# Performance work log

Measured on AMD Instinct MI355X. Metric: run time of the kernel, lower is better.

Reference implementation:

```python
import jax, jax.numpy as jnp
import numpy as np

EMBED_DIM = 768
NUM_HEADS = 12
LORA_DIM = 64
HEAD_DIM = EMBED_DIM // NUM_HEADS
SCALING = float(HEAD_DIM) ** -0.5


def quick_gelu(x):
    return x * jax.nn.sigmoid(1.702 * x)


def setup_inputs() -> dict:
    key = jax.random.key(0)
    ks = jax.random.split(key, 12)
    bsz, tgt_len, E = 128, 197, EMBED_DIM
    x = jax.random.normal(ks[0], (bsz, tgt_len, E), dtype=jnp.float32)
    attn_mask = jnp.zeros((bsz, tgt_len, tgt_len), dtype=jnp.float32)
    top_idx = jax.random.randint(ks[1], (bsz,), 0, tgt_len)
    s = 0.02
    return {
        "x": x,
        "attn_mask": attn_mask,
        "in_proj_weight": jax.random.normal(ks[2], (3 * E, E)) * s,
        "in_proj_bias": jnp.zeros((3 * E,), jnp.float32),
        "out_proj_weight": jax.random.normal(ks[3], (E, E)) * s,
        "out_proj_bias": jnp.zeros((E,), jnp.float32),
        "lora_a": jax.random.normal(ks[4], (LORA_DIM, E)) * s,
        "lora_b": jax.random.normal(ks[5], (3 * E, LORA_DIM)) * s,
        "down_weight": jax.random.normal(ks[6], (LORA_DIM, E)) * s,
        "down_bias": jax.random.normal(ks[7], (LORA_DIM,)) * 1e-6,
        "up_weight": jax.random.normal(ks[8], (E, LORA_DIM)) * s,
        "up_bias": jnp.zeros((E,), jnp.float32),
        "n_f": 16,
        "top_idx": top_idx,
    }


def reference(x, attn_mask, in_proj_weight, in_proj_bias, out_proj_weight,
              out_proj_bias, lora_a, lora_b, down_weight, down_bias,
              up_weight, up_bias, n_f, top_idx):
    bsz, tgt_len, E = x.shape
    H, hd = NUM_HEADS, HEAD_DIM
    b = bsz // n_f

    # fused QKV + LoRA delta
    qkv = x @ in_proj_weight.T + in_proj_bias          # [bsz, L, 3E]
    qkv = qkv + (x @ lora_a.T) @ lora_b.T              # LoRA delta
    qkv = qkv.reshape(bsz, tgt_len, 3, H, hd)
    qkv = jnp.transpose(qkv, (2, 0, 3, 1, 4))          # [3, bsz, H, L, hd]
    q, k, v = qkv[0], qkv[1], qkv[2]

    # gather per-sample CLS query before scaling (matches torch order)
    q_1 = q[jnp.arange(bsz), :, top_idx, :]            # [bsz, H, hd]
    q_1 = jnp.transpose(q_1.reshape(b, n_f, H, hd), (0, 2, 1, 3))  # [b, H, f, hd]

    # frame-local attention
    attn = jnp.einsum('bhqd,bhkd->bhqk', q * SCALING, k) + attn_mask[:, None, :, :]
    attn = jax.nn.softmax(attn, axis=-1)
    xo = jnp.einsum('bhqk,bhkd->bhqd', attn, v)
    xo = jnp.transpose(xo, (0, 2, 1, 3)).reshape(bsz, tgt_len, E)
    xo = xo @ out_proj_weight.T + out_proj_bias        # [bsz, L, E]

    # global CLS attention over all frames' keys/values
    k_g = jnp.transpose(k.reshape(b, n_f, H, tgt_len, hd), (0, 2, 1, 3, 4)).reshape(b, H, n_f * tgt_len, hd)
    v_g = jnp.transpose(v.reshape(b, n_f, H, tgt_len, hd), (0, 2, 1, 3, 4)).reshape(b, H, n_f * tgt_len, hd)
    mask_g = attn_mask[:, -1, :].reshape(b, n_f * tgt_len)  # [b, f*L]

    attn_1 = jnp.einsum('bhfd,bhkd->bhfk', q_1 * SCALING, k_g) + mask_g[:, None, None, :]
    attn_1 = jax.nn.softmax(attn_1, axis=-1)
    x_1 = jnp.einsum('bhfk,bhkd->bhfd', attn_1, v_g)
    x_1 = jnp.transpose(x_1, (0, 2, 1, 3)).reshape(b, n_f, E)
    x_1 = x_1 @ out_proj_weight.T + out_proj_bias      # [b, f, E]

    # adapter on gathered CLS outputs
    x_0 = xo[jnp.arange(bsz), top_idx, :].reshape(b, n_f, E)
    x_0 = quick_gelu(x_0 @ down_weight.T + down_bias)
    x_0 = x_0 @ up_weight.T + up_bias                  # [b, f, E]

    update_cls = (x_0 + x_1).reshape(bsz, E)
    xo = xo.at[jnp.arange(bsz), top_idx, :].set(update_cls)
    return xo
```

## Files before the change

kernel.cpp:

```cpp
#include <hip/hip_runtime.h>
#include <hip/hip_bf16.h>

typedef __attribute__((ext_vector_type(4))) float f32x4;
typedef __attribute__((ext_vector_type(8))) short s16x8;

#define BSZ 128
#define TGT 197
#define EDIM 768
#define NH 12
#define HD 64
#define NF 16
#define M_TOT (BSZ*TGT)
#define QKV_N (3*EDIM)
#define KG (NF*TGT)
#define KGP 3328
#define VSTR 264

__device__ __forceinline__ float b2f(unsigned short u) {
  return __uint_as_float(((unsigned int)u) << 16);
}
__device__ __forceinline__ float bf2f(__hip_bfloat16 b) { return __bfloat162float(b); }
__device__ __forceinline__ __hip_bfloat16 f2bf(float f) { return __float2bfloat16(f); }
__device__ __forceinline__ unsigned int packbf(float a, float b) {
  __hip_bfloat16 x = __float2bfloat16(a), y = __float2bfloat16(b);
  return (unsigned int)*(unsigned short*)&x | ((unsigned int)*(unsigned short*)&y << 16);
}
__device__ __forceinline__ int swz(int t, int c) {
  return t*64 + (c ^ ((((t & 7) ^ ((t >> 3) & 3))) << 3));
}
__device__ __forceinline__ int vswz(int d, int t) {
  return d*VSTR + (t ^ (d & 56));
}

__device__ __forceinline__ void gload_lds16(const void* gsrc, void* ldst) {
  __builtin_amdgcn_global_load_lds(
      (const __attribute__((address_space(1))) unsigned int*)gsrc,
      (__attribute__((address_space(3))) unsigned int*)ldst, 16, 0, 0);
}

__global__ void detect_dtype(const unsigned short* __restrict__ xraw,
                             int* __restrict__ flag, int* __restrict__ mz) {
  if (threadIdx.x == 0 && blockIdx.x == 0) {
    float mx = 0.f;
    for (int j = 0; j < 1024; ++j) {
      float v = fabsf(b2f(xraw[j]));
      if (v < 1e30f) mx = fmaxf(mx, v);
      else mx = 1e30f;
    }
    *flag = (mx < 100.0f) ? 1 : 0;
    *mz = 1;
  }
}

__global__ __launch_bounds__(256) void detect_mask_zero(
    const unsigned int* __restrict__ mraw, int nelem,
    const int* __restrict__ flag, int* __restrict__ mz)
{
  const int isbf = *flag;
  const int nwords = isbf ? (nelem >> 1) : nelem;
  const unsigned int am = isbf ? 0x7fff7fffu : 0x7fffffffu;
  unsigned int acc = 0;
  for (int i = blockIdx.x*256 + threadIdx.x; i < nwords; i += gridDim.x*256)
    acc |= (mraw[i] & am);
  if (acc) atomicAnd(mz, 0);
}

__global__ __launch_bounds__(256) void convert_bf16(
    const void* __restrict__ src, __hip_bfloat16* __restrict__ dst,
    int n8, const int* __restrict__ flag, int skip_if_bf)
{
  const int isbf = *flag;
  if (skip_if_bf && isbf) return;
  int i = blockIdx.x * 256 + threadIdx.x;
  const int stride = gridDim.x * 256;
  if (isbf) {
    const s16x8* s = (const s16x8*)src;
    s16x8* d = (s16x8*)dst;
    for (; i < n8; i += stride) d[i] = s[i];
  } else {
    const f32x4* s = (const f32x4*)src;
    s16x8* d = (s16x8*)dst;
    for (; i < n8; i += stride) {
      f32x4 a = s[i*2], b = s[i*2+1];
      s16x8 o;
      #pragma unroll
      for (int j = 0; j < 4; ++j) { __hip_bfloat16 t = f2bf(a[j]); o[j] = *(short*)&t; }
      #pragma unroll
      for (int j = 0; j < 4; ++j) { __hip_bfloat16 t = f2bf(b[j]); o[4+j] = *(short*)&t; }
      d[i] = o;
    }
  }
}

__global__ __launch_bounds__(256) void build_wc(
    const __hip_bfloat16* __restrict__ W,
    const __hip_bfloat16* __restrict__ la,
    const __hip_bfloat16* __restrict__ lb,
    __hip_bfloat16* __restrict__ Wc)
{
  __shared__ float lbr[64];
  const int n = blockIdx.x;
  if (threadIdx.x < 64) lbr[threadIdx.x] = bf2f(lb[n*64 + threadIdx.x]);
  __syncthreads();
  for (int e = threadIdx.x; e < EDIM; e += 256) {
    float acc = bf2f(W[(size_t)n*EDIM + e]);
    for (int r = 0; r < 64; ++r) acc += lbr[r] * bf2f(la[r*EDIM + e]);
    Wc[(size_t)n*EDIM + e] = f2bf(acc);
  }
}

__global__ __launch_bounds__(512) void gemm_bt_8ph(
    const __hip_bfloat16* __restrict__ A,
    const __hip_bfloat16* __restrict__ A_alt,
    const __hip_bfloat16* __restrict__ B,
    const __hip_bfloat16* __restrict__ bias,
    void* __restrict__ C,
    int M, int N, int K, int ntiles,
    const int* __restrict__ flag, int flag_mode)
{
  __shared__ char lds[131072];
  const int tid = threadIdx.x;
  const int wave = tid >> 6, lane = tid & 63;
  const int l16 = lane & 15, kq = lane >> 4;
  const int wr = wave >> 2, wc2 = wave & 3;

  const int nwg = gridDim.x;
  const int bid = blockIdx.x;
  const int qc = nwg >> 3, rc = nwg & 7;
  const int xcd = bid & 7;
  const int wgid = (xcd < rc ? xcd*(qc+1) : rc*(qc+1) + (xcd-rc)*qc) + (bid >> 3);
  const long brow = (long)(wgid / ntiles) * 256;
  const long bcol = (long)(wgid % ntiles) * 256;

  const int isbf = *flag;
  const __hip_bfloat16* Ause = isbf ? A_alt : A;
  const int nkt = K >> 6;

  const int srow = tid >> 3;
  const int schunk = tid & 7;
  const int wuni = wave << 10;

  auto stA = [&](int t, int buf, int issue) {
    int ar = issue*64 + srow;
    int cs = schunk ^ (ar & 7);
    long gr = brow + ar; if (gr > (long)M - 1) gr = M - 1;
    gload_lds16(Ause + gr*(long)K + t*64 + cs*8,
                lds + buf*65536 + issue*8192 + wuni);
  };
  auto stB = [&](int t, int buf, int issue) {
    int br = issue*64 + srow;
    int cs = schunk ^ (br & 7);
    gload_lds16(B + (bcol + br)*(long)K + t*64 + cs*8,
                lds + buf*65536 + 32768 + issue*8192 + wuni);
  };
  auto rdA = [&](int buf, int q, int a, int ks) -> s16x8 {
    int ar = wr*128 + q*32 + a*16 + l16;
    int ch = ks*4 + kq;
    return *(const s16x8*)(lds + buf*65536 + ar*128 + ((ch ^ (ar & 7)) << 4));
  };
  auto rdB = [&](int buf, int ni, int ks) -> s16x8 {
    int br = wc2*64 + ni*16 + l16;
    int ch = ks*4 + kq;
    return *(const s16x8*)(lds + buf*65536 + 32768 + br*128 + ((ch ^ (br & 7)) << 4));
  };

  f32x4 acc[8][4];
  #pragma unroll
  for (int i = 0; i < 8; ++i)
    #pragma unroll
    for (int j = 0; j < 4; ++j) acc[i][j] = (f32x4){0.f,0.f,0.f,0.f};

  stB(0,0,0); stB(0,0,1); stB(0,0,2); stB(0,0,3);
  stA(0,0,0); stA(0,0,2); stA(0,0,1); stA(0,0,3);
  asm volatile("s_waitcnt vmcnt(2)" ::: "memory");
  __builtin_amdgcn_s_barrier();

  for (int t = 0; t < nkt; ++t) {
    const int cur = t & 1, nxt = cur ^ 1;
    const bool pf = (t + 1 < nkt);
    s16x8 bfr[4][2], af[2][2];

    #pragma unroll
    for (int ni = 0; ni < 4; ++ni) { bfr[ni][0] = rdB(cur,ni,0); bfr[ni][1] = rdB(cur,ni,1); }
    af[0][0]=rdA(cur,0,0,0); af[0][1]=rdA(cur,0,0,1);
    af[1][0]=rdA(cur,0,1,0); af[1][1]=rdA(cur,0,1,1);
    if (pf) { stB(t+1,nxt,0); stB(t+1,nxt,1); }
    __builtin_amdgcn_s_barrier();
    asm volatile("s_waitcnt lgkmcnt(0)" ::: "memory");
    __builtin_amdgcn_sched_barrier(0);
    __builtin_amdgcn_s_setprio(1);
    #pragma unroll
    for (int ks = 0; ks < 2; ++ks)
      #pragma unroll
      for (int ni = 0; ni < 4; ++ni) {
        acc[0][ni] = __builtin_amdgcn_mfma_f32_16x16x32_bf16(af[0][ks], bfr[ni][ks], acc[0][ni], 0,0,0);
        acc[1][ni] = __builtin_amdgcn_mfma_f32_16x16x32_bf16(af[1][ks], bfr[ni][ks], acc[1][ni], 0,0,0);
      }
    __builtin_amdgcn_s_setprio(0);

    af[0][0]=rdA(cur,1,0,0); af[0][1]=rdA(cur,1,0,1);
    af[1][0]=rdA(cur,1,1,0); af[1][1]=rdA(cur,1,1,1);
    if (pf) {
      stB(t+1,nxt,2); stB(t+1,nxt,3);
      asm volatile("s_waitcnt vmcnt(4)" ::: "memory");
    } else {
      asm volatile("s_waitcnt vmcnt(0)" ::: "memory");
    }
    __builtin_amdgcn_s_barrier();
    asm volatile("s_waitcnt lgkmcnt(0)" ::: "memory");
    __builtin_amdgcn_sched_barrier(0);
    __builtin_amdgcn_s_setprio(1);
    #pragma unroll
    for (int ks = 0; ks < 2; ++ks)
      #pragma unroll
      for (int ni = 0; ni < 4; ++ni) {
        acc[2][ni] = __builtin_amdgcn_mfma_f32_16x16x32_bf16(af[0][ks], bfr[ni][ks], acc[2][ni], 0,0,0);
        acc[3][ni] = __builtin_amdgcn_mfma_f32_16x16x32_bf16(af[1][ks], bfr[ni][ks], acc[3][ni], 0,0,0);
      }
    __builtin_amdgcn_s_setprio(0);

    af[0][0]=rdA(cur,2,0,0); af[0][1]=rdA(cur,2,0,1);
    af[1][0]=rdA(cur,2,1,0); af[1][1]=rdA(cur,2,1,1);
    if (pf) { stA(t+1,nxt,0); stA(t+1,nxt,2); }
    __builtin_amdgcn_s_barrier();
    asm volatile("s_waitcnt lgkmcnt(0)" ::: "memory");
    __builtin_amdgcn_sched_barrier(0);
    __builtin_amdgcn_s_setprio(1);
    #pragma unroll
    for (int ks = 0; ks < 2; ++ks)
      #pragma unroll
      for (int ni = 0; ni < 4; ++ni) {
        acc[4][ni] = __builtin_amdgcn_mfma_f32_16x16x32_bf16(af[0][ks], bfr[ni][ks], acc[4][ni], 0,0,0);
        acc[5][ni] = __builtin_amdgcn_mfma_f32_16x16x32_bf16(af[1][ks], bfr[ni][ks], acc[5][ni], 0,0,0);
      }
    __builtin_amdgcn_s_setprio(0);

    af[0][0]=rdA(cur,3,0,0); af[0][1]=rdA(cur,3,0,1);
    af[1][0]=rdA(cur,3,1,0); af[1][1]=rdA(cur,3,1,1);
    if (pf) { stA(t+1,nxt,1); stA(t+1,nxt,3); }
    asm volatile("s_waitcnt vmcnt(2)" ::: "memory");
    __builtin_amdgcn_s_barrier();
    asm volatile("s_waitcnt lgkmcnt(0)" ::: "memory");
    __builtin_amdgcn_sched_barrier(0);
    __builtin_amdgcn_s_setprio(1);
    #pragma unroll
    for (int ks = 0; ks < 2; ++ks)
      #pragma unroll
      for (int ni = 0; ni < 4; ++ni) {
        acc[6][ni] = __builtin_amdgcn_mfma_f32_16x16x32_bf16(af[0][ks], bfr[ni][ks], acc[6][ni], 0,0,0);
        acc[7][ni] = __builtin_amdgcn_mfma_f32_16x16x32_bf16(af[1][ks], bfr[ni][ks], acc[7][ni], 0,0,0);
      }
    __builtin_amdgcn_s_setprio(0);
  }

  __builtin_amdgcn_s_barrier();

  const int f32o = flag_mode && (!isbf);
  float bv[4];
  #pragma unroll
  for (int ni = 0; ni < 4; ++ni) bv[ni] = bf2f(bias[bcol + wc2*64 + ni*16 + l16]);
  const int o4 = kq*4;

  if (!f32o) {
    __hip_bfloat16* eb = (__hip_bfloat16*)(lds + wave*2048);
    __hip_bfloat16* Cb = (__hip_bfloat16*)C;
    const int rr = lane >> 3, cg = lane & 7;
    #pragma unroll
    for (int mi = 0; mi < 8; ++mi) {
      #pragma unroll
      for (int ni = 0; ni < 4; ++ni)
        #pragma unroll
        for (int r = 0; r < 4; ++r) {
          const int row16 = o4 + r;
          const int sidx = row16*64 + ((((ni*2 + (l16 >> 3)) ^ (row16 & 7)) << 3) | (l16 & 7));
          eb[sidx] = f2bf(acc[mi][ni][r] + bv[ni]);
        }
      asm volatile("s_waitcnt lgkmcnt(0)" ::: "memory");
      __builtin_amdgcn_sched_barrier(0);
      #pragma unroll
      for (int pass = 0; pass < 2; ++pass) {
        const int row16 = pass*8 + rr;
        const long grow = brow + wr*128 + mi*16 + row16;
        if (grow < M) {
          s16x8 v = *(const s16x8*)(eb + row16*64 + ((cg ^ (row16 & 7)) << 3));
          *(s16x8*)(Cb + grow*(long)N + bcol + wc2*64 + cg*8) = v;
        }
      }
      asm volatile("s_waitcnt lgkmcnt(0)" ::: "memory");
      __builtin_amdgcn_sched_barrier(0);
    }
  } else {
    #pragma unroll
    for (int mi = 0; mi < 8; ++mi)
      #pragma unroll
      for (int ni = 0; ni < 4; ++ni)
        #pragma unroll
        for (int r = 0; r < 4; ++r) {
          const long grow = brow + wr*128 + mi*16 + o4 + r;
          if (grow < M)
            ((float*)C)[grow*(long)N + bcol + wc2*64 + ni*16 + l16] = acc[mi][ni][r] + bv[ni];
        }
  }
}

__global__ __launch_bounds__(256) void attn_fused(
    const __hip_bfloat16* __restrict__ qkv,
    const __hip_bfloat16* __restrict__ mask,
    const __hip_bfloat16* __restrict__ mask_raw,
    const int* __restrict__ flag,
    const int* __restrict__ mzp,
    __hip_bfloat16* __restrict__ xop)
{
  __shared__ __hip_bfloat16 lVt[64*VSTR];

  const int tid = threadIdx.x;
  const int blk = blockIdx.x;
  const int xcd = blk & 7;
  const int slot = blk >> 3;
  const int ih = xcd * 192 + (slot >> 2);
  const int qt = slot & 3;
  const int h = ih % NH;
  const int i = ih / NH;
  const int q0 = qt * 64;
  const size_t rowbase = (size_t)i * TGT;
  const int wave = tid >> 6, lane = tid & 63;
  const int l16 = lane & 15, kq = lane >> 4;
  const int mz = *mzp;
  const __hip_bfloat16* msk = (*flag) ? mask_raw : mask;

  int qr = q0 + wave*16 + l16;
  const int qrc = qr > TGT-1 ? TGT-1 : qr;
  s16x8 qf[2];
  #pragma unroll
  for (int kk = 0; kk < 2; ++kk)
    qf[kk] = *(const s16x8*)(qkv + (rowbase + qrc)*QKV_N + h*HD + kk*32 + kq*8);

  const f32x4 z = {0.f,0.f,0.f,0.f};
  for (int idx = tid; idx < 224*8; idx += 256) {
    int t = idx >> 3, c8 = idx & 7;
    f32x4 vv = z;
    if (t < TGT) vv = *(const f32x4*)(qkv + (rowbase + t)*QKV_N + 2*EDIM + h*HD + c8*8);
    const __hip_bfloat16* pv = (const __hip_bfloat16*)&vv;
    const int tx = t ^ (c8 << 3);
    #pragma unroll
    for (int j = 0; j < 8; ++j)
      lVt[(c8*8 + j)*VSTR + tx] = pv[j];
  }
  __syncthreads();

  f32x4 acc[14];
  #pragma unroll
  for (int nf = 0; nf < 14; ++nf) {
    int trow = nf*16 + l16; if (trow > TGT-1) trow = TGT-1;
    acc[nf] = (f32x4){0.f,0.f,0.f,0.f};
    #pragma unroll
    for (int kk = 0; kk < 2; ++kk) {
      s16x8 kf = *(const s16x8*)(qkv + (rowbase + trow)*QKV_N + EDIM + h*HD + kk*32 + kq*8);
      acc[nf] = __builtin_amdgcn_mfma_f32_16x16x32_bf16(kf, qf[kk], acc[nf], 0, 0, 0);
    }
  }

  float mx = -1e30f;
  #pragma unroll
  for (int nf = 0; nf < 14; ++nf) {
    #pragma unroll
    for (int r = 0; r < 4; ++r) {
      const int t = nf*16 + kq*4 + r;
      float s;
      if (t < TGT) {
        s = acc[nf][r]*0.125f;
        if (!mz) s += bf2f(msk[(rowbase + qrc)*TGT + t]);
      } else s = -1e30f;
      acc[nf][r] = s;
      mx = fmaxf(mx, s);
    }
  }
  mx = fmaxf(mx, __shfl_xor(mx, 16));
  mx = fmaxf(mx, __shfl_xor(mx, 32));

  float rs = 0.f;
  unsigned int pk[14][2];
  #pragma unroll
  for (int nf = 0; nf < 14; ++nf) {
    float p0 = __expf(acc[nf][0] - mx);
    float p1 = __expf(acc[nf][1] - mx);
    float p2 = __expf(acc[nf][2] - mx);
    float p3 = __expf(acc[nf][3] - mx);
    rs += (p0 + p1) + (p2 + p3);
    pk[nf][0] = packbf(p0, p1);
    pk[nf][1] = packbf(p2, p3);
  }
  rs += __shfl_xor(rs, 16);
  rs += __shfl_xor(rs, 32);

  f32x4 oacc[4];
  #pragma unroll
  for (int nf = 0; nf < 4; ++nf) oacc[nf] = (f32x4){0.f,0.f,0.f,0.f};

  const int slbase = l16 + ((kq & 1) << 5);
  #pragma unroll
  for (int kt = 0; kt < 7; ++kt) {
    s16x8 pa;
    #pragma unroll
    for (int jp = 0; jp < 4; ++jp) {
      const int srcLane = slbase + ((jp >> 1) << 4);
      int va = __shfl((int)pk[2*kt][jp & 1], srcLane, 64);
      int vb = __shfl((int)pk[2*kt + 1][jp & 1], srcLane, 64);
      int sel = (kq < 2) ? va : vb;
      pa[2*jp]     = (short)(sel & 0xffff);
      pa[2*jp + 1] = (short)(((unsigned int)sel) >> 16);
    }
    #pragma unroll
    for (int nf = 0; nf < 4; ++nf) {
      s16x8 vf = *(const s16x8*)(lVt + vswz(nf*16 + l16, kt*32 + kq*8));
      oacc[nf] = __builtin_amdgcn_mfma_f32_16x16x32_bf16(pa, vf, oacc[nf], 0, 0, 0);
    }
  }

  #pragma unroll
  for (int r = 0; r < 4; ++r) {
    const float rsrc = __shfl(rs, kq*4 + r, 64);
    const int qw = q0 + wave*16 + kq*4 + r;
    if (qw < TGT) {
      const float inv = 1.0f / rsrc;
      #pragma unroll
      for (int nf = 0; nf < 4; ++nf)
        xop[(rowbase + qw)*(size_t)EDIM + h*HD + nf*16 + l16] = f2bf(oacc[nf][r] * inv);
    }
  }
}

__global__ __launch_bounds__(256) void cls_attn(
    const __hip_bfloat16* __restrict__ qkv,
    const __hip_bfloat16* __restrict__ mask,
    const __hip_bfloat16* __restrict__ mask_raw,
    const int* __restrict__ flag,
    const int* __restrict__ mzp,
    const int* __restrict__ top_idx,
    __hip_bfloat16* __restrict__ Sg_all,
    __hip_bfloat16* __restrict__ x1buf)
{
  __shared__ __hip_bfloat16 lQ[16*64];
  __shared__ __hip_bfloat16 lV[256*64];
  __shared__ float red[16][17];
  __shared__ float rmax[16];
  __shared__ float rsum[16];

  const int tid = threadIdx.x;
  const int g = blockIdx.x / NH;
  const int h = blockIdx.x % NH;
  __hip_bfloat16* Sg = Sg_all + (size_t)blockIdx.x * 16 * KGP;
  const int wave = tid >> 6, lane = tid & 63;
  const int l16 = lane & 15, kq = lane >> 4, o4 = (lane >> 4) * 4;
  const int mz = *mzp;
  const __hip_bfloat16* msk = (*flag) ? mask_raw : mask;

  if (tid < 128) {
    int qi = tid >> 3, c8 = tid & 7;
    int ib = g*NF + qi;
    int top = top_idx[ib];
    f32x4 v = *(const f32x4*)(qkv + ((size_t)ib*TGT + top)*QKV_N + h*HD + c8*8);
    *(f32x4*)(lQ + qi*64 + c8*8) = v;
  }
  __syncthreads();

  s16x8 q8[2];
  #pragma unroll
  for (int kk = 0; kk < 2; ++kk)
    q8[kk] = *(const s16x8*)(lQ + l16*64 + kk*32 + kq*8);

  for (int nf = wave; nf < 208; nf += 4) {
    const int key = nf*16 + l16;
    if (nf < 197) {
      f32x4 a = {0.f,0.f,0.f,0.f};
      const size_t krow = (size_t)g*KG + key;
      #pragma unroll
      for (int kk = 0; kk < 2; ++kk) {
        s16x8 k8 = *(const s16x8*)(qkv + krow*QKV_N + EDIM + h*HD + kk*32 + kq*8);
        a = __builtin_amdgcn_mfma_f32_16x16x32_bf16(q8[kk], k8, a, 0, 0, 0);
      }
      float mval = 0.f;
      if (!mz) {
        const int f = key / 197;
        const int t = key - f*197;
        mval = bf2f(msk[((size_t)(g*NF + f)*TGT + (TGT-1))*TGT + t]);
      }
      #pragma unroll
      for (int r = 0; r < 4; ++r)
        Sg[(o4 + r)*KGP + key] = f2bf(a[r]*0.125f + mval);
    } else {
      #pragma unroll
      for (int r = 0; r < 4; ++r)
        Sg[(o4 + r)*KGP + key] = f2bf(0.f);
    }
  }
  __syncthreads();

  {
    const int q = tid >> 4, c = tid & 15;
    float mx = -1e30f;
    for (int gch = c; gch < 394; gch += 16) {
      s16x8 sv = *(const s16x8*)(Sg + q*KGP + gch*8);
      #pragma unroll
      for (int j = 0; j < 8; ++j) mx = fmaxf(mx, b2f((unsigned short)sv[j]));
    }
    red[q][c] = mx;
    __syncthreads();
    if (tid < 16) {
      float m = red[tid][0];
      for (int j = 1; j < 16; ++j) m = fmaxf(m, red[tid][j]);
      rmax[tid] = m;
    }
    __syncthreads();
    const float rowmax = rmax[q];
    float sum = 0.f;
    for (int gch = c; gch < 394; gch += 16) {
      s16x8 sv = *(const s16x8*)(Sg + q*KGP + gch*8);
      s16x8 ov;
      #pragma unroll
      for (int jp = 0; jp < 4; ++jp) {
        float e0 = __expf(b2f((unsigned short)sv[2*jp])   - rowmax);
        float e1 = __expf(b2f((unsigned short)sv[2*jp+1]) - rowmax);
        sum += e0 + e1;
        unsigned int pr = packbf(e0, e1);
        ov[2*jp]   = (short)(pr & 0xffff);
        ov[2*jp+1] = (short)(pr >> 16);
      }
      *(s16x8*)(Sg + q*KGP + gch*8) = ov;
    }
    red[q][c] = sum;
    __syncthreads();
    if (tid < 16) {
      float s = 0.f;
      for (int j = 0; j < 16; ++j) s += red[tid][j];
      rsum[tid] = s;
    }
  }

  f32x4 oa = {0.f,0.f,0.f,0.f};
  const f32x4 z = {0.f,0.f,0.f,0.f};
  for (int ck = 0; ck < KGP; ck += 256) {
    __syncthreads();
    for (int idx = tid; idx < 256*8; idx += 256) {
      int t2 = idx >> 3, c8 = idx & 7;
      int key = ck + t2;
      f32x4 v = z;
      if (key < KG) v = *(const f32x4*)(qkv + ((size_t)g*KG + key)*QKV_N + 2*EDIM + h*HD + c8*8);
      *(f32x4*)(lV + swz(t2, c8*8)) = v;
    }
    __syncthreads();
    #pragma unroll
    for (int ks = 0; ks < 8; ++ks) {
      s16x8 pa = *(const s16x8*)(Sg + l16*KGP + ck + ks*32 + kq*8);
      s16x8 vf;
      #pragma unroll
      for (int j = 0; j < 8; ++j) {
        const int t2 = ks*32 + kq*8 + j;
        vf[j] = *(const short*)(lV + swz(t2, wave*16 + l16));
      }
      oa = __builtin_amdgcn_mfma_f32_16x16x32_bf16(pa, vf, oa, 0, 0, 0);
    }
  }
  #pragma unroll
  for (int r = 0; r < 4; ++r) {
    int q = o4 + r;
    int ib = g*NF + q;
    x1buf[(size_t)ib*EDIM + h*HD + wave*16 + l16] = f2bf(oa[r] / rsum[q]);
  }
}

__global__ __launch_bounds__(256) void final_update(
    void* __restrict__ out,
    const __hip_bfloat16* __restrict__ x1p,
    const __hip_bfloat16* __restrict__ dw, const __hip_bfloat16* __restrict__ db,
    const __hip_bfloat16* __restrict__ uw, const __hip_bfloat16* __restrict__ ub,
    const int* __restrict__ top_idx, const int* __restrict__ flag)
{
  __shared__ float x0[EDIM];
  __shared__ float hmid[64];
  const int i = blockIdx.x;
  const int tid = threadIdx.x;
  const int top = top_idx[i];
  const int isbf = *flag;
  const size_t rowoff = ((size_t)i*TGT + top)*EDIM;
  for (int e = tid; e < EDIM; e += 256)
    x0[e] = isbf ? bf2f(((const __hip_bfloat16*)out)[rowoff + e])
                 : ((const float*)out)[rowoff + e];
  __syncthreads();
  if (tid < 64) {
    float a = bf2f(db[tid]);
    for (int e = 0; e < EDIM; ++e) a += x0[e] * bf2f(dw[tid*EDIM + e]);
    hmid[tid] = a / (1.f + __expf(-1.702f * a));
  }
  __syncthreads();
  for (int e = tid; e < EDIM; e += 256) {
    float a = bf2f(ub[e]) + bf2f(x1p[(size_t)i*EDIM + e]);
    #pragma unroll
    for (int r = 0; r < 64; ++r) a += hmid[r] * bf2f(uw[e*64 + r]);
    if (isbf) ((__hip_bfloat16*)out)[rowoff + e] = f2bf(a);
    else ((float*)out)[rowoff + e] = a;
  }
}

extern "C" void kernel_launch(void* const* d_in, const int* in_sizes, int n_in,
                              void* d_out, int out_size, void* d_ws, size_t ws_size,
                              hipStream_t stream) {
  (void)in_sizes; (void)n_in; (void)out_size; (void)ws_size;
  const int* top_idx = (const int*)d_in[13];
  const __hip_bfloat16* x_raw    = (const __hip_bfloat16*)d_in[0];
  const __hip_bfloat16* mask_raw = (const __hip_bfloat16*)d_in[1];

  char* ws = (char*)d_ws;
  size_t off = 0;
  auto alloc = [&](size_t bytes) { char* p = ws + off; off += (bytes + 15) & ~(size_t)15; return p; };

  int* flag = (int*)alloc(16);
  int* mz   = (int*)alloc(16);
  __hip_bfloat16* x_c    = (__hip_bfloat16*)alloc((size_t)19365888*2);
  __hip_bfloat16* mask_c = (__hip_bfloat16*)alloc((size_t)4967552*2);
  __hip_bfloat16* wIn_c  = (__hip_bfloat16*)alloc((size_t)1769472*2);
  __hip_bfloat16* bIn_c  = (__hip_bfloat16*)alloc((size_t)2304*2);
  __hip_bfloat16* wOut_c = (__hip_bfloat16*)alloc((size_t)589824*2);
  __hip_bfloat16* bOut_c = (__hip_bfloat16*)alloc((size_t)768*2);
  __hip_bfloat16* la_c   = (__hip_bfloat16*)alloc((size_t)49152*2);
  __hip_bfloat16* lb_c   = (__hip_bfloat16*)alloc((size_t)147456*2);
  __hip_bfloat16* dw_c   = (__hip_bfloat16*)alloc((size_t)49152*2);
  __hip_bfloat16* db_c   = (__hip_bfloat16*)alloc((size_t)64*2);
  __hip_bfloat16* uw_c   = (__hip_bfloat16*)alloc((size_t)49152*2);
  __hip_bfloat16* ub_c   = (__hip_bfloat16*)alloc((size_t)768*2);
  __hip_bfloat16* Wc     = (__hip_bfloat16*)alloc((size_t)QKV_N*EDIM*2);
  __hip_bfloat16* qkv    = (__hip_bfloat16*)alloc((size_t)M_TOT*QKV_N*2);
  __hip_bfloat16* xop    = (__hip_bfloat16*)alloc((size_t)M_TOT*EDIM*2);
  __hip_bfloat16* x1b    = (__hip_bfloat16*)alloc((size_t)BSZ*EDIM*2);
  __hip_bfloat16* x1p    = (__hip_bfloat16*)alloc((size_t)BSZ*EDIM*2);
  __hip_bfloat16* Sg     = (__hip_bfloat16*)alloc((size_t)96*16*KGP*2);

  detect_dtype<<<1, 64, 0, stream>>>((const unsigned short*)d_in[0], flag, mz);
  detect_mask_zero<<<2048, 256, 0, stream>>>((const unsigned int*)d_in[1], 4967552, flag, mz);

  auto CV = [&](int idx, __hip_bfloat16* dst, int n, int skip) {
    int n8 = n / 8;
    int grid = (n8 + 255) / 256; if (grid > 2048) grid = 2048; if (grid < 1) grid = 1;
    convert_bf16<<<grid, 256, 0, stream>>>(d_in[idx], dst, n8, flag, skip);
  };
  CV(0,  x_c,    19365888, 1);
  CV(1,  mask_c, 4967552, 1);
  CV(2,  wIn_c,  1769472, 0);
  CV(3,  bIn_c,  2304, 0);
  CV(4,  wOut_c, 589824, 0);
  CV(5,  bOut_c, 768, 0);
  CV(6,  la_c,   49152, 0);
  CV(7,  lb_c,   147456, 0);
  CV(8,  dw_c,   49152, 0);
  CV(9,  db_c,   64, 0);
  CV(10, uw_c,   49152, 0);
  CV(11, ub_c,   768, 0);

  build_wc<<<2304, 256, 0, stream>>>(wIn_c, la_c, lb_c, Wc);

  gemm_bt_8ph<<<99*9, 512, 0, stream>>>(x_c, x_raw, Wc, bIn_c, qkv,
                                        M_TOT, QKV_N, EDIM, 9, flag, 0);
  attn_fused<<<dim3(6144), 256, 0, stream>>>(qkv, mask_c, mask_raw, flag, mz, xop);
  gemm_bt_8ph<<<99*3, 512, 0, stream>>>(xop, xop, wOut_c, bOut_c, d_out,
                                        M_TOT, EDIM, EDIM, 3, flag, 1);
  cls_attn<<<dim3(96), 256, 0, stream>>>(qkv, mask_c, mask_raw, flag, mz, top_idx, Sg, x1b);
  gemm_bt_8ph<<<1*3, 512, 0, stream>>>(x1b, x1b, wOut_c, bOut_c, x1p,
                                       BSZ, EDIM, EDIM, 3, flag, 0);
  final_update<<<128, 256, 0, stream>>>(d_out, x1p, dw_c, db_c, uw_c, ub_c, top_idx, flag);
}
```

Measured before the change: 569.4 us.

## Batch small weight conversions into one launch and issue all GEMM prefetches up front

```diff
diff --git a/kernel.cpp b/kernel.cpp
--- a/kernel.cpp
+++ b/kernel.cpp
@@ -88,6 +88,36 @@
       #pragma unroll
       for (int j = 0; j < 4; ++j) { __hip_bfloat16 t = f2bf(b[j]); o[4+j] = *(short*)&t; }
       d[i] = o;
+    }
+  }
+}
+
+struct CvBatch {
+  const void* src[10];
+  void* dst[10];
+  int off8[11];
+};
+
+__global__ __launch_bounds__(256) void convert_batch(CvBatch cb, const int* __restrict__ flag)
+{
+  const int isbf = *flag;
+  const int total = cb.off8[10];
+  for (int i = blockIdx.x*256 + threadIdx.x; i < total; i += gridDim.x*256) {
+    int s = 0;
+    #pragma unroll
+    for (int k = 1; k < 10; ++k) s += (i >= cb.off8[k]);
+    const int li = i - cb.off8[s];
+    if (isbf) {
+      ((s16x8*)cb.dst[s])[li] = ((const s16x8*)cb.src[s])[li];
+    } else {
+      const f32x4* sp = (const f32x4*)cb.src[s];
+      f32x4 a = sp[li*2], b = sp[li*2+1];
+      s16x8 o;
+      #pragma unroll
+      for (int j = 0; j < 4; ++j) { __hip_bfloat16 t = f2bf(a[j]); o[j] = *(short*)&t; }
+      #pragma unroll
+      for (int j = 0; j < 4; ++j) { __hip_bfloat16 t = f2bf(b[j]); o[4+j] = *(short*)&t; }
+      ((s16x8*)cb.dst[s])[li] = o;
     }
   }
 }
@@ -184,7 +214,10 @@
     for (int ni = 0; ni < 4; ++ni) { bfr[ni][0] = rdB(cur,ni,0); bfr[ni][1] = rdB(cur,ni,1); }
     af[0][0]=rdA(cur,0,0,0); af[0][1]=rdA(cur,0,0,1);
     af[1][0]=rdA(cur,0,1,0); af[1][1]=rdA(cur,0,1,1);
-    if (pf) { stB(t+1,nxt,0); stB(t+1,nxt,1); }
+    if (pf) {
+      stB(t+1,nxt,0); stB(t+1,nxt,1); stB(t+1,nxt,2); stB(t+1,nxt,3);
+      stA(t+1,nxt,0); stA(t+1,nxt,2); stA(t+1,nxt,1); stA(t+1,nxt,3);
+    }
     __builtin_amdgcn_s_barrier();
     asm volatile("s_waitcnt lgkmcnt(0)" ::: "memory");
     __builtin_amdgcn_sched_barrier(0);
@@ -200,12 +233,8 @@
 
     af[0][0]=rdA(cur,1,0,0); af[0][1]=rdA(cur,1,0,1);
     af[1][0]=rdA(cur,1,1,0); af[1][1]=rdA(cur,1,1,1);
-    if (pf) {
-      stB(t+1,nxt,2); stB(t+1,nxt,3);
-      asm volatile("s_waitcnt vmcnt(4)" ::: "memory");
-    } else {
-      asm volatile("s_waitcnt vmcnt(0)" ::: "memory");
-    }
+    if (pf) asm volatile("s_waitcnt vmcnt(8)" ::: "memory");
+    else    asm volatile("s_waitcnt vmcnt(0)" ::: "memory");
     __builtin_amdgcn_s_barrier();
     asm volatile("s_waitcnt lgkmcnt(0)" ::: "memory");
     __builtin_amdgcn_sched_barrier(0);
@@ -221,7 +250,6 @@
 
     af[0][0]=rdA(cur,2,0,0); af[0][1]=rdA(cur,2,0,1);
     af[1][0]=rdA(cur,2,1,0); af[1][1]=rdA(cur,2,1,1);
-    if (pf) { stA(t+1,nxt,0); stA(t+1,nxt,2); }
     __builtin_amdgcn_s_barrier();
     asm volatile("s_waitcnt lgkmcnt(0)" ::: "memory");
     __builtin_amdgcn_sched_barrier(0);
@@ -237,8 +265,7 @@
 
     af[0][0]=rdA(cur,3,0,0); af[0][1]=rdA(cur,3,0,1);
     af[1][0]=rdA(cur,3,1,0); af[1][1]=rdA(cur,3,1,1);
-    if (pf) { stA(t+1,nxt,1); stA(t+1,nxt,3); }
-    asm volatile("s_waitcnt vmcnt(2)" ::: "memory");
+    if (pf) asm volatile("s_waitcnt vmcnt(2)" ::: "memory");
     __builtin_amdgcn_s_barrier();
     asm volatile("s_waitcnt lgkmcnt(0)" ::: "memory");
     __builtin_amdgcn_sched_barrier(0);
@@ -638,23 +665,22 @@
   detect_dtype<<<1, 64, 0, stream>>>((const unsigned short*)d_in[0], flag, mz);
   detect_mask_zero<<<2048, 256, 0, stream>>>((const unsigned int*)d_in[1], 4967552, flag, mz);
 
-  auto CV = [&](int idx, __hip_bfloat16* dst, int n, int skip) {
-    int n8 = n / 8;
-    int grid = (n8 + 255) / 256; if (grid > 2048) grid = 2048; if (grid < 1) grid = 1;
-    convert_bf16<<<grid, 256, 0, stream>>>(d_in[idx], dst, n8, flag, skip);
-  };
-  CV(0,  x_c,    19365888, 1);
-  CV(1,  mask_c, 4967552, 1);
-  CV(2,  wIn_c,  1769472, 0);
-  CV(3,  bIn_c,  2304, 0);
-  CV(4,  wOut_c, 589824, 0);
-  CV(5,  bOut_c, 768, 0);
-  CV(6,  la_c,   49152, 0);
-  CV(7,  lb_c,   147456, 0);
-  CV(8,  dw_c,   49152, 0);
-  CV(9,  db_c,   64, 0);
-  CV(10, uw_c,   49152, 0);
-  CV(11, ub_c,   768, 0);
+  convert_bf16<<<2048, 256, 0, stream>>>(d_in[0], x_c, 19365888/8, flag, 1);
+  convert_bf16<<<2048, 256, 0, stream>>>(d_in[1], mask_c, 4967552/8, flag, 1);
+
+  CvBatch cb;
+  const int srcIdx[10] = {2,3,4,5,6,7,8,9,10,11};
+  void* dsts[10] = {wIn_c, bIn_c, wOut_c, bOut_c, la_c, lb_c, dw_c, db_c, uw_c, ub_c};
+  const int ns[10] = {1769472, 2304, 589824, 768, 49152, 147456, 49152, 64, 49152, 768};
+  int cum = 0;
+  for (int k = 0; k < 10; ++k) {
+    cb.src[k] = d_in[srcIdx[k]];
+    cb.dst[k] = dsts[k];
+    cb.off8[k] = cum;
+    cum += ns[k] / 8;
+  }
+  cb.off8[10] = cum;
+  convert_batch<<<(cum + 255)/256, 256, 0, stream>>>(cb, flag);
 
   build_wc<<<2304, 256, 0, stream>>>(wIn_c, la_c, lb_c, Wc);
 
```

After: 561.9 us. No clear change (-1.3%).
